# Performance work log

Hardware: AMD Instinct MI355X
Metric: run time of the kernel (lower is better)

## Reference

```python
import jax, jax.numpy as jnp
import numpy as np

B, HF, WF = 16, 32, 32
DIM, NH = 1024, 16
HD = DIM // NH  # 64


def axial_freqs(H, W, head_dim):
    # RotaryEmbedding(dim=head_dim//4, freqs_for='pixel', max_freq=H*W)
    d = head_dim // 4  # rotary dim per axis
    base = jnp.linspace(1.0, (H * W) / 2.0, d // 2) * jnp.pi  # [d//2]
    posH = jnp.linspace(-1.0, 1.0, H)
    posW = jnp.linspace(-1.0, 1.0, W)
    fH = jnp.repeat(posH[:, None] * base[None, :], 2, axis=-1)  # [H, d]
    fW = jnp.repeat(posW[:, None] * base[None, :], 2, axis=-1)  # [W, d]
    fH = jnp.broadcast_to(fH[:, None, :], (H, W, d))
    fW = jnp.broadcast_to(fW[None, :, :], (H, W, d))
    return jnp.concatenate([fH, fW], axis=-1)  # [H, W, 2d] = [H, W, head_dim//2]


def rotate_half(x):
    # interleaved pair rotation: (x1, x2) -> (-x2, x1)
    xr = x.reshape(*x.shape[:-1], -1, 2)
    x1, x2 = xr[..., 0], xr[..., 1]
    return jnp.stack([-x2, x1], axis=-1).reshape(x.shape)


def apply_rotary(freqs, t):
    # t: [B, h, H, W, hd]; freqs: [H, W, rot_dim]
    rd = freqs.shape[-1]
    t_rot, t_pass = t[..., :rd], t[..., rd:]
    t_rot = t_rot * jnp.cos(freqs) + rotate_half(t_rot) * jnp.sin(freqs)
    return jnp.concatenate([t_rot, t_pass], axis=-1)


def setup_inputs() -> dict:
    key = jax.random.key(0)
    k1, k2, k3 = jax.random.split(key, 3)
    s = 1.0 / np.sqrt(DIM)
    return {
        "x": jax.random.normal(k1, (B, HF * WF, DIM), jnp.float32),
        "w_qkv": jax.random.normal(k2, (3 * DIM, DIM), jnp.float32) * s,
        "w_proj": jax.random.normal(k3, (DIM, DIM), jnp.float32) * s,
        "b_proj": jnp.zeros((DIM,), jnp.float32),
    }


def reference(x, w_qkv, w_proj, b_proj):
    freqs = axial_freqs(HF, WF, HD)
    qkv = x @ w_qkv.T  # [B, N, 3*DIM]
    q, k, v = jnp.split(qkv, 3, axis=-1)

    def to_grid(t):  # [B, N, DIM] -> [B, h, H, W, hd]
        return t.reshape(B, HF, WF, NH, HD).transpose(0, 3, 1, 2, 4)

    q, k, v = to_grid(q), to_grid(k), to_grid(v)
    q = apply_rotary(freqs, q)
    k = apply_rotary(freqs, k)
    N = HF * WF
    q = q.reshape(B, NH, N, HD)
    k = k.reshape(B, NH, N, HD)
    v = v.reshape(B, NH, N, HD)

    scale = 1.0 / np.sqrt(HD)
    attn = jax.nn.softmax(jnp.einsum('bhnd,bhmd->bhnm', q, k) * scale, axis=-1)
    out = jnp.einsum('bhnm,bhmd->bhnd', attn, v)  # [B, h, N, hd]
    out = out.transpose(0, 2, 1, 3).reshape(B, N, DIM)
    return out @ w_proj.T + b_proj
```

## Files before the change

kernel.cpp:

```cpp
#include <hip/hip_runtime.h>
#include <hip/hip_bf16.h>
#include <math.h>

typedef __bf16 bf16;
typedef bf16 bf16x2 __attribute__((ext_vector_type(2)));
typedef bf16 bf16x4 __attribute__((ext_vector_type(4)));
typedef bf16 bf16x8 __attribute__((ext_vector_type(8)));
typedef float f32x4 __attribute__((ext_vector_type(4)));
typedef float f32x16 __attribute__((ext_vector_type(16)));
typedef unsigned int uint;
typedef uint uint32x4 __attribute__((ext_vector_type(4)));

#define MFMA16(a, b, c) __builtin_amdgcn_mfma_f32_16x16x32_bf16((a), (b), (c), 0, 0, 0)
#define MFMA32(a, b, c) __builtin_amdgcn_mfma_f32_32x32x16_bf16((a), (b), (c), 0, 0, 0)

#define QSCALE 0.18033688011112042f

__device__ __forceinline__ void async16(const void* g, void* l) {
  __builtin_amdgcn_global_load_lds(
      (const __attribute__((address_space(1))) void*)g,
      (__attribute__((address_space(3))) void*)l, 16, 0, 0);
}

__device__ __forceinline__ uint pkbf(float a, float b) {
  bf16x2 t = {(bf16)a, (bf16)b};
  return __builtin_bit_cast(uint, t);
}

__device__ __forceinline__ void pls(uint& x, uint& y) {
  asm volatile("v_permlane32_swap_b32 %0, %1" : "+v"(x), "+v"(y));
}

__global__ __launch_bounds__(256) void f2b_all_kernel(const float* __restrict__ x,
                                                      const float* __restrict__ wqkv,
                                                      const float* __restrict__ wproj,
                                                      bf16* __restrict__ xb,
                                                      bf16* __restrict__ wqb,
                                                      bf16* __restrict__ wpb) {
  int t = blockIdx.x * 256 + threadIdx.x;
  const float* in;
  bf16* out;
  int i;
  if (t < 4194304) {
    in = x; out = xb; i = t * 4;
  } else if (t < 4980736) {
    in = wqkv; out = wqb; i = (t - 4194304) * 4;
  } else {
    in = wproj; out = wpb; i = (t - 4980736) * 4;
  }
  f32x4 v = *(const f32x4*)(in + i);
  bf16x4 o = {(bf16)v[0], (bf16)v[1], (bf16)v[2], (bf16)v[3]};
  *(bf16x4*)(out + i) = o;
}

__global__ __launch_bounds__(256) void table_kernel(float* __restrict__ cosT,
                                                    float* __restrict__ sinT) {
  int idx = blockIdx.x * 256 + threadIdx.x;
  if (idx >= 1024 * 32) return;
  int n = idx >> 5, d = idx & 31;
  int hf = n >> 5, wf = n & 31;
  int bi = (d & 15) >> 1;
  float base = (1.0f + 73.0f * bi) * 3.14159265358979323846f;
  int p = (d < 16) ? hf : wf;
  float pos = (2.0f * (float)p - 31.0f) * (1.0f / 31.0f);
  float f = pos * base;
  cosT[idx] = cosf(f);
  sinT[idx] = sinf(f);
}

template <int EPI, int NBN>
__global__ __launch_bounds__(512, 2) void gemm_bt(
    const bf16* __restrict__ A, const bf16* __restrict__ W,
    bf16* __restrict__ oq, bf16* __restrict__ okk, bf16* __restrict__ ovt,
    const float* __restrict__ cosT, const float* __restrict__ sinT,
    float* __restrict__ outF, const float* __restrict__ bias) {
  constexpr int K = 1024;
  __shared__ bf16 As[4][256 * 32];
  __shared__ bf16 Bs[4][256 * 32];

  const int tid = threadIdx.x;
  const int lane = tid & 63;
  const int wid = tid >> 6;
  const int lo = lane & 15, hi = lane >> 4;
  const int wm = wid >> 2;
  const int wn = wid & 3;

  const int wg = blockIdx.x;
  const int xcd = wg & 7;
  const int i = wg >> 3;
  const int s = i >> 4;
  const int r = i & 15;
  const int bm = xcd * 8 + (s & 1) * 4 + (r & 3);
  const int bn = (s >> 1) * 4 + (r >> 2);

  const bf16* Ab = A + (size_t)bm * 256 * K;
  const bf16* Wb = W + (size_t)bn * 256 * K;

  const f32x4 fzero = {0.f, 0.f, 0.f, 0.f};
  f32x4 acc[8][4];
#pragma unroll
  for (int i2 = 0; i2 < 8; ++i2)
#pragma unroll
    for (int j = 0; j < 4; ++j) acc[i2][j] = fzero;

  size_t srcOff[2];
  int ldsOff[2];
#pragma unroll
  for (int i2 = 0; i2 < 2; ++i2) {
    const int c = i2 * 512 + tid;
    const int row = c >> 2, g = c & 3;
    const int gsrc = g ^ ((row >> 1) & 3);
    srcOff[i2] = (size_t)row * K + gsrc * 8;
    ldsOff[i2] = c * 8;
  }

  auto stageSlot = [&](int slot, int kh) {
#pragma unroll
    for (int i2 = 0; i2 < 2; ++i2)
      async16(Ab + srcOff[i2] + kh * 32, &As[slot][ldsOff[i2]]);
#pragma unroll
    for (int i2 = 0; i2 < 2; ++i2)
      async16(Wb + srcOff[i2] + kh * 32, &Bs[slot][ldsOff[i2]]);
  };

  auto compute = [&](int slot) {
    bf16x8 af[8], bf[4];
#pragma unroll
    for (int mf = 0; mf < 8; ++mf) {
      const int row = wm * 128 + mf * 16 + lo;
      const int g = hi ^ ((row >> 1) & 3);
      af[mf] = *(const bf16x8*)&As[slot][row * 32 + g * 8];
    }
#pragma unroll
    for (int nf = 0; nf < 4; ++nf) {
      const int row = wn * 64 + nf * 16 + lo;
      const int g = hi ^ ((row >> 1) & 3);
      bf[nf] = *(const bf16x8*)&Bs[slot][row * 32 + g * 8];
    }
    __builtin_amdgcn_s_setprio(1);
#pragma unroll
    for (int mf = 0; mf < 8; ++mf)
#pragma unroll
      for (int nf = 0; nf < 4; ++nf)
        acc[mf][nf] = MFMA16(af[mf], bf[nf], acc[mf][nf]);
    __builtin_amdgcn_s_setprio(0);
  };

  stageSlot(0, 0);
  stageSlot(1, 1);

  for (int kt = 0; kt < 7; ++kt) {
#pragma unroll
    for (int ph = 0; ph < 4; ++ph) {
      stageSlot((ph + 2) & 3, kt * 4 + ph + 2);
      asm volatile("s_waitcnt vmcnt(8)" ::: "memory");
      __builtin_amdgcn_s_barrier();
      compute(ph);
    }
  }
  stageSlot(2, 30);
  asm volatile("s_waitcnt vmcnt(8)" ::: "memory");
  __builtin_amdgcn_s_barrier();
  compute(0);
  stageSlot(3, 31);
  asm volatile("s_waitcnt vmcnt(8)" ::: "memory");
  __builtin_amdgcn_s_barrier();
  compute(1);
  asm volatile("s_waitcnt vmcnt(4)" ::: "memory");
  __builtin_amdgcn_s_barrier();
  compute(2);
  asm volatile("s_waitcnt vmcnt(0)" ::: "memory");
  __builtin_amdgcn_s_barrier();
  compute(3);

  const int rb0 = bm * 256 + wm * 128;
  const int jb0 = bn * 256 + wn * 64;

  if constexpr (EPI == 0) {
#pragma unroll
    for (int ac = 0; ac < 4; ++ac) {
      const int j = jb0 + ac * 16 + lo;
      const int which = j >> 10;
      const int f = j & 1023;
      const int h = f >> 6, d = f & 63;
#pragma unroll
      for (int ar = 0; ar < 8; ++ar) {
        const int rb = rb0 + ar * 16 + 4 * hi;
        f32x4 v = acc[ar][ac];
        if (which == 2) {
          const int b = rb >> 10, n0 = rb & 1023;
          bf16x4 pk = {(bf16)v[0], (bf16)v[1], (bf16)v[2], (bf16)v[3]};
          *(bf16x4*)(ovt + ((size_t)((b * 16 + h) * 64 + d)) * 1024 + n0) = pk;
        } else {
          bf16* dst = which ? okk : oq;
          const float sc = which ? 1.0f : QSCALE;
#pragma unroll
          for (int reg = 0; reg < 4; ++reg) {
            const int r2 = rb + reg;
            const int b = r2 >> 10, n = r2 & 1023;
            float val = v[reg];
            float res;
            if (d < 32) {
              float c = cosT[n * 32 + d];
              float sn = sinT[n * 32 + d];
              float pp = __shfl_xor(val, 1);
              res = (d & 1) ? fmaf(val, c, pp * sn) : fmaf(val, c, -(pp * sn));
            } else {
              res = val;
            }
            dst[((size_t)((b * 16 + h) * 1024 + n)) * 64 + d] = (bf16)(res * sc);
          }
        }
      }
    }
  } else {
#pragma unroll
    for (int ac = 0; ac < 4; ++ac) {
      const int j = jb0 + ac * 16 + lo;
      const float bv = bias[j];
#pragma unroll
      for (int ar = 0; ar < 8; ++ar) {
        const int rb = rb0 + ar * 16 + 4 * hi;
#pragma unroll
        for (int reg = 0; reg < 4; ++reg)
          outF[(size_t)(rb + reg) * 1024 + j] = acc[ar][ac][reg] + bv;
      }
    }
  }
}

__global__ __launch_bounds__(512, 4) void attn_fwd(const bf16* __restrict__ q,
                                                   const bf16* __restrict__ k,
                                                   const bf16* __restrict__ vt,
                                                   bf16* __restrict__ o) {
  __shared__ bf16 Kt[2][64 * 64];
  __shared__ bf16 Vt[2][64 * 64];
  __shared__ float Psm[8][32];
  const int tid = threadIdx.x;
  const int lane = tid & 63, wid = tid >> 6;
  const int l31 = lane & 31;
  const int s = lane >> 5;
  const int m7 = l31 & 7;
  const int j = blockIdx.x;
  const int bh = (j & 7) + ((j >> 5) << 3);
  const int qt = (j >> 3) & 3;
  const bf16* qg = q + (size_t)bh * 65536;
  const bf16* kg = k + (size_t)bh * 65536;
  const bf16* vg = vt + (size_t)bh * 65536;

  const int qrow = qt * 256 + wid * 32 + l31;
  bf16x8 qf[4];
#pragma unroll
  for (int kb4 = 0; kb4 < 4; ++kb4)
    qf[kb4] = *(const bf16x8*)(qg + (size_t)qrow * 64 + kb4 * 16 + s * 8);

  const int srow = tid >> 3;
  const int sgsrc = (tid & 7) ^ (srow & 7);
  auto stageKV = [&](int buf, int kv) {
    async16(kg + (size_t)(kv * 64 + srow) * 64 + sgsrc * 8, &Kt[buf][tid * 8]);
    async16(vg + (size_t)srow * 1024 + kv * 64 + sgsrc * 8, &Vt[buf][tid * 8]);
  };

  asm volatile("s_waitcnt vmcnt(0)" ::: "memory");
  stageKV(0, 0);

  f32x16 of0 = {0.f, 0.f, 0.f, 0.f, 0.f, 0.f, 0.f, 0.f,
                0.f, 0.f, 0.f, 0.f, 0.f, 0.f, 0.f, 0.f};
  f32x16 of1 = of0;
  float psum = 0.f;

  for (int kv = 0; kv < 16; ++kv) {
    const int cur = kv & 1;
    if (kv < 15) {
      stageKV(cur ^ 1, kv + 1);
      asm volatile("s_waitcnt vmcnt(2)" ::: "memory");
    } else {
      asm volatile("s_waitcnt vmcnt(0)" ::: "memory");
    }
    __builtin_amdgcn_s_barrier();

    f32x16 z0 = {0.f, 0.f, 0.f, 0.f, 0.f, 0.f, 0.f, 0.f,
                 0.f, 0.f, 0.f, 0.f, 0.f, 0.f, 0.f, 0.f};
    f32x16 z1 = z0;
#pragma unroll
    for (int kb4 = 0; kb4 < 4; ++kb4) {
      bf16x8 k0 = *(const bf16x8*)&Kt[cur][l31 * 64 + (((2 * kb4 + s) ^ m7) * 8)];
      bf16x8 k1 = *(const bf16x8*)&Kt[cur][(32 + l31) * 64 + (((2 * kb4 + s) ^ m7) * 8)];
      z0 = MFMA32(k0, qf[kb4], z0);
      z1 = MFMA32(k1, qf[kb4], z1);
    }

    uint c0[8], c1[8];
#pragma unroll
    for (int m = 0; m < 8; ++m) {
      float a0 = __builtin_amdgcn_exp2f(z0[2 * m]);
      float b0 = __builtin_amdgcn_exp2f(z0[2 * m + 1]);
      float a1 = __builtin_amdgcn_exp2f(z1[2 * m]);
      float b1 = __builtin_amdgcn_exp2f(z1[2 * m + 1]);
      psum += (a0 + b0) + (a1 + b1);
      c0[m] = pkbf(a0, b0);
      c1[m] = pkbf(a1, b1);
    }

    auto pv = [&](uint* cc, int bb, int kb) {
      uint w0 = cc[4 * bb], w2 = cc[4 * bb + 2];
      uint w1 = cc[4 * bb + 1], w3 = cc[4 * bb + 3];
      pls(w0, w2);
      pls(w1, w3);
      uint32x4 W = {w0, w1, w2, w3};
      bf16x8 apv = __builtin_bit_cast(bf16x8, W);
      bf16x8 vb0 = *(const bf16x8*)&Vt[cur][l31 * 64 + (((2 * kb + s) ^ m7) * 8)];
      bf16x8 vb1 = *(const bf16x8*)&Vt[cur][(32 + l31) * 64 + (((2 * kb + s) ^ m7) * 8)];
      of0 = MFMA32(apv, vb0, of0);
      of1 = MFMA32(apv, vb1, of1);
    };
    pv(c0, 0, 0);
    pv(c0, 1, 1);
    pv(c1, 0, 2);
    pv(c1, 1, 3);

    __syncthreads();
  }

  psum += __shfl_xor(psum, 32);
  const float inv = 1.0f / psum;
  if (lane < 32) Psm[wid][l31] = inv;
  __syncthreads();

  const int b = bh >> 4, h = bh & 15;
#pragma unroll
  for (int r = 0; r < 16; ++r) {
    const int qr = (r & 3) + 8 * (r >> 2) + 4 * s;
    const float iv = Psm[wid][qr];
    const int n = qt * 256 + wid * 32 + qr;
    const size_t base = ((size_t)(b * 1024 + n)) * 1024 + h * 64 + l31;
    o[base] = (bf16)(of0[r] * iv);
    o[base + 32] = (bf16)(of1[r] * iv);
  }
}

extern "C" void kernel_launch(void* const* d_in, const int* in_sizes, int n_in,
                              void* d_out, int out_size, void* d_ws, size_t ws_size,
                              hipStream_t stream) {
  (void)in_sizes; (void)n_in; (void)out_size; (void)ws_size;
  const float* x = (const float*)d_in[0];
  const float* wqkv = (const float*)d_in[1];
  const float* wproj = (const float*)d_in[2];
  const float* bproj = (const float*)d_in[3];

  char* ws = (char*)d_ws;
  bf16* xb = (bf16*)(ws);
  bf16* wqb = (bf16*)(ws + 33554432);
  bf16* wpb = (bf16*)(ws + 39845888);
  float* cosT = (float*)(ws + 41943040);
  float* sinT = (float*)(ws + 42074112);
  bf16* qb = (bf16*)(ws + 42205184);
  bf16* kb = (bf16*)(ws + 75759616);
  bf16* vtb = (bf16*)(ws + 109314048);

  f2b_all_kernel<<<20480, 256, 0, stream>>>(x, wqkv, wproj, xb, wqb, wpb);
  table_kernel<<<128, 256, 0, stream>>>(cosT, sinT);

  gemm_bt<0, 12><<<768, 512, 0, stream>>>(xb, wqb, qb, kb, vtb, cosT, sinT,
                                          nullptr, nullptr);
  attn_fwd<<<1024, 512, 0, stream>>>(qb, kb, vtb, xb);
  gemm_bt<1, 4><<<256, 512, 0, stream>>>(xb, wpb, nullptr, nullptr, nullptr,
                                         nullptr, nullptr, (float*)d_out, bproj);
}
```

Baseline: 253.8 us.

## Switch GEMM mainloop to double-buffered BK=64 stages with wider swizzle

Replaces the four-slot, 32-wide K pipeline (prefetch distance 2) with two 64-wide K slots and a prefetch distance of 1. Each stage now issues twice as many async loads and runs two MFMA sub-steps, and the LDS XOR swizzle is changed to an 8-group pattern. There are half as many barrier phases, but a second barrier is added per iteration to guard slot reuse. Less load-latency hiding is the risk. The shared-memory footprint stays the same.

```diff
diff --git a/kernel.cpp b/kernel.cpp
--- a/kernel.cpp
+++ b/kernel.cpp
@@ -75,8 +75,8 @@
     const float* __restrict__ cosT, const float* __restrict__ sinT,
     float* __restrict__ outF, const float* __restrict__ bias) {
   constexpr int K = 1024;
-  __shared__ bf16 As[4][256 * 32];
-  __shared__ bf16 Bs[4][256 * 32];
+  __shared__ bf16 As[2][256 * 64];
+  __shared__ bf16 Bs[2][256 * 64];
 
   const int tid = threadIdx.x;
   const int lane = tid & 63;
@@ -88,10 +88,10 @@
   const int wg = blockIdx.x;
   const int xcd = wg & 7;
   const int i = wg >> 3;
-  const int s = i >> 4;
-  const int r = i & 15;
-  const int bm = xcd * 8 + (s & 1) * 4 + (r & 3);
-  const int bn = (s >> 1) * 4 + (r >> 2);
+  const int s4 = i >> 4;
+  const int r4 = i & 15;
+  const int bm = xcd * 8 + (s4 & 1) * 4 + (r4 & 3);
+  const int bn = (s4 >> 1) * 4 + (r4 >> 2);
 
   const bf16* Ab = A + (size_t)bm * 256 * K;
   const bf16* Wb = W + (size_t)bn * 256 * K;
@@ -103,75 +103,64 @@
 #pragma unroll
     for (int j = 0; j < 4; ++j) acc[i2][j] = fzero;
 
-  size_t srcOff[2];
-  int ldsOff[2];
-#pragma unroll
-  for (int i2 = 0; i2 < 2; ++i2) {
+  size_t srcOff[4];
+  int ldsOff[4];
+#pragma unroll
+  for (int i2 = 0; i2 < 4; ++i2) {
     const int c = i2 * 512 + tid;
-    const int row = c >> 2, g = c & 3;
-    const int gsrc = g ^ ((row >> 1) & 3);
+    const int row = c >> 3, g = c & 7;
+    const int gsrc = g ^ (row & 7);
     srcOff[i2] = (size_t)row * K + gsrc * 8;
     ldsOff[i2] = c * 8;
   }
 
-  auto stageSlot = [&](int slot, int kh) {
-#pragma unroll
-    for (int i2 = 0; i2 < 2; ++i2)
-      async16(Ab + srcOff[i2] + kh * 32, &As[slot][ldsOff[i2]]);
-#pragma unroll
-    for (int i2 = 0; i2 < 2; ++i2)
-      async16(Wb + srcOff[i2] + kh * 32, &Bs[slot][ldsOff[i2]]);
+  auto stageSlot = [&](int slot, int kt) {
+#pragma unroll
+    for (int i2 = 0; i2 < 4; ++i2)
+      async16(Ab + srcOff[i2] + kt * 64, &As[slot][ldsOff[i2]]);
+#pragma unroll
+    for (int i2 = 0; i2 < 4; ++i2)
+      async16(Wb + srcOff[i2] + kt * 64, &Bs[slot][ldsOff[i2]]);
   };
 
   auto compute = [&](int slot) {
-    bf16x8 af[8], bf[4];
-#pragma unroll
-    for (int mf = 0; mf < 8; ++mf) {
-      const int row = wm * 128 + mf * 16 + lo;
-      const int g = hi ^ ((row >> 1) & 3);
-      af[mf] = *(const bf16x8*)&As[slot][row * 32 + g * 8];
-    }
-#pragma unroll
-    for (int nf = 0; nf < 4; ++nf) {
-      const int row = wn * 64 + nf * 16 + lo;
-      const int g = hi ^ ((row >> 1) & 3);
-      bf[nf] = *(const bf16x8*)&Bs[slot][row * 32 + g * 8];
-    }
-    __builtin_amdgcn_s_setprio(1);
-#pragma unroll
-    for (int mf = 0; mf < 8; ++mf)
-#pragma unroll
-      for (int nf = 0; nf < 4; ++nf)
-        acc[mf][nf] = MFMA16(af[mf], bf[nf], acc[mf][nf]);
-    __builtin_amdgcn_s_setprio(0);
+#pragma unroll
+    for (int s = 0; s < 2; ++s) {
+      bf16x8 af[8], bf[4];
+#pragma unroll
+      for (int mf = 0; mf < 8; ++mf) {
+        const int row = wm * 128 + mf * 16 + lo;
+        const int g = (s * 4 + hi) ^ (row & 7);
+        af[mf] = *(const bf16x8*)&As[slot][row * 64 + g * 8];
+      }
+#pragma unroll
+      for (int nf = 0; nf < 4; ++nf) {
+        const int row = wn * 64 + nf * 16 + lo;
+        const int g = (s * 4 + hi) ^ (row & 7);
+        bf[nf] = *(const bf16x8*)&Bs[slot][row * 64 + g * 8];
+      }
+      __builtin_amdgcn_s_setprio(1);
+#pragma unroll
+      for (int mf = 0; mf < 8; ++mf)
+#pragma unroll
+        for (int nf = 0; nf < 4; ++nf)
+          acc[mf][nf] = MFMA16(af[mf], bf[nf], acc[mf][nf]);
+      __builtin_amdgcn_s_setprio(0);
+    }
   };
 
   stageSlot(0, 0);
-  stageSlot(1, 1);
-
-  for (int kt = 0; kt < 7; ++kt) {
-#pragma unroll
-    for (int ph = 0; ph < 4; ++ph) {
-      stageSlot((ph + 2) & 3, kt * 4 + ph + 2);
-      asm volatile("s_waitcnt vmcnt(8)" ::: "memory");
-      __builtin_amdgcn_s_barrier();
-      compute(ph);
-    }
-  }
-  stageSlot(2, 30);
-  asm volatile("s_waitcnt vmcnt(8)" ::: "memory");
-  __builtin_amdgcn_s_barrier();
-  compute(0);
-  stageSlot(3, 31);
-  asm volatile("s_waitcnt vmcnt(8)" ::: "memory");
+
+  for (int p = 0; p < 15; ++p) {
+    stageSlot((p + 1) & 1, p + 1);
+    asm volatile("s_waitcnt vmcnt(8)" ::: "memory");
+    __builtin_amdgcn_s_barrier();
+    compute(p & 1);
+    __builtin_amdgcn_s_barrier();
+  }
+  asm volatile("s_waitcnt vmcnt(0)" ::: "memory");
   __builtin_amdgcn_s_barrier();
   compute(1);
-  asm volatile("s_waitcnt vmcnt(4)" ::: "memory");
-  __builtin_amdgcn_s_barrier();
-  compute(2);
-  asm volatile("s_waitcnt vmcnt(0)" ::: "memory");
-  __builtin_amdgcn_s_barrier();
-  compute(3);
 
   const int rb0 = bm * 256 + wm * 128;
   const int jb0 = bn * 256 + wn * 64;
```

After: 264.3 us. +4.1%, slower.

## Process 64 query rows per wave in attention to reuse K/V tiles

Applied to the files above, without the earlier changes.

Each wave in the attention kernel now handles two 32-row query slices instead of one, so every K and V fragment read from LDS feeds twice as many MFMAs. The grid is halved to 512 blocks of 512 query rows, which halves the global K/V staging traffic per query. In exchange register use roughly doubles (launch bounds lowered to 2 blocks per CU), occupancy drops, and fewer blocks are available to fill the GPU.

```diff
diff --git a/kernel.cpp b/kernel.cpp
--- a/kernel.cpp
+++ b/kernel.cpp
@@ -229,30 +229,33 @@
   }
 }
 
-__global__ __launch_bounds__(512, 4) void attn_fwd(const bf16* __restrict__ q,
+__global__ __launch_bounds__(512, 2) void attn_fwd(const bf16* __restrict__ q,
                                                    const bf16* __restrict__ k,
                                                    const bf16* __restrict__ vt,
                                                    bf16* __restrict__ o) {
   __shared__ bf16 Kt[2][64 * 64];
   __shared__ bf16 Vt[2][64 * 64];
-  __shared__ float Psm[8][32];
+  __shared__ float Psm[8][64];
   const int tid = threadIdx.x;
   const int lane = tid & 63, wid = tid >> 6;
   const int l31 = lane & 31;
   const int s = lane >> 5;
   const int m7 = l31 & 7;
   const int j = blockIdx.x;
-  const int bh = (j & 7) + ((j >> 5) << 3);
-  const int qt = (j >> 3) & 3;
+  const int bh = (j & 7) + ((j >> 4) << 3);
+  const int qt = (j >> 3) & 1;
   const bf16* qg = q + (size_t)bh * 65536;
   const bf16* kg = k + (size_t)bh * 65536;
   const bf16* vg = vt + (size_t)bh * 65536;
 
-  const int qrow = qt * 256 + wid * 32 + l31;
-  bf16x8 qf[4];
-#pragma unroll
-  for (int kb4 = 0; kb4 < 4; ++kb4)
-    qf[kb4] = *(const bf16x8*)(qg + (size_t)qrow * 64 + kb4 * 16 + s * 8);
+  bf16x8 qf[2][4];
+#pragma unroll
+  for (int rs = 0; rs < 2; ++rs) {
+    const int qrow = qt * 512 + wid * 64 + rs * 32 + l31;
+#pragma unroll
+    for (int kb4 = 0; kb4 < 4; ++kb4)
+      qf[rs][kb4] = *(const bf16x8*)(qg + (size_t)qrow * 64 + kb4 * 16 + s * 8);
+  }
 
   const int srow = tid >> 3;
   const int sgsrc = (tid & 7) ^ (srow & 7);
@@ -264,10 +267,10 @@
   asm volatile("s_waitcnt vmcnt(0)" ::: "memory");
   stageKV(0, 0);
 
-  f32x16 of0 = {0.f, 0.f, 0.f, 0.f, 0.f, 0.f, 0.f, 0.f,
-                0.f, 0.f, 0.f, 0.f, 0.f, 0.f, 0.f, 0.f};
-  f32x16 of1 = of0;
-  float psum = 0.f;
+  const f32x16 z16 = {0.f, 0.f, 0.f, 0.f, 0.f, 0.f, 0.f, 0.f,
+                      0.f, 0.f, 0.f, 0.f, 0.f, 0.f, 0.f, 0.f};
+  f32x16 of00 = z16, of01 = z16, of10 = z16, of11 = z16;
+  float psum0 = 0.f, psum1 = 0.f;
 
   for (int kv = 0; kv < 16; ++kv) {
     const int cur = kv & 1;
@@ -279,63 +282,84 @@
     }
     __builtin_amdgcn_s_barrier();
 
-    f32x16 z0 = {0.f, 0.f, 0.f, 0.f, 0.f, 0.f, 0.f, 0.f,
-                 0.f, 0.f, 0.f, 0.f, 0.f, 0.f, 0.f, 0.f};
-    f32x16 z1 = z0;
+    f32x16 z00 = z16, z01 = z16, z10 = z16, z11 = z16;
 #pragma unroll
     for (int kb4 = 0; kb4 < 4; ++kb4) {
       bf16x8 k0 = *(const bf16x8*)&Kt[cur][l31 * 64 + (((2 * kb4 + s) ^ m7) * 8)];
       bf16x8 k1 = *(const bf16x8*)&Kt[cur][(32 + l31) * 64 + (((2 * kb4 + s) ^ m7) * 8)];
-      z0 = MFMA32(k0, qf[kb4], z0);
-      z1 = MFMA32(k1, qf[kb4], z1);
-    }
-
-    uint c0[8], c1[8];
+      z00 = MFMA32(k0, qf[0][kb4], z00);
+      z01 = MFMA32(k1, qf[0][kb4], z01);
+      z10 = MFMA32(k0, qf[1][kb4], z10);
+      z11 = MFMA32(k1, qf[1][kb4], z11);
+    }
+
+    uint c00[8], c01[8], c10[8], c11[8];
 #pragma unroll
     for (int m = 0; m < 8; ++m) {
-      float a0 = __builtin_amdgcn_exp2f(z0[2 * m]);
-      float b0 = __builtin_amdgcn_exp2f(z0[2 * m + 1]);
-      float a1 = __builtin_amdgcn_exp2f(z1[2 * m]);
-      float b1 = __builtin_amdgcn_exp2f(z1[2 * m + 1]);
-      psum += (a0 + b0) + (a1 + b1);
-      c0[m] = pkbf(a0, b0);
-      c1[m] = pkbf(a1, b1);
-    }
-
-    auto pv = [&](uint* cc, int bb, int kb) {
-      uint w0 = cc[4 * bb], w2 = cc[4 * bb + 2];
-      uint w1 = cc[4 * bb + 1], w3 = cc[4 * bb + 3];
+      float a, b;
+      a = __builtin_amdgcn_exp2f(z00[2 * m]); b = __builtin_amdgcn_exp2f(z00[2 * m + 1]);
+      psum0 += a + b; c00[m] = pkbf(a, b);
+      a = __builtin_amdgcn_exp2f(z01[2 * m]); b = __builtin_amdgcn_exp2f(z01[2 * m + 1]);
+      psum0 += a + b; c01[m] = pkbf(a, b);
+      a = __builtin_amdgcn_exp2f(z10[2 * m]); b = __builtin_amdgcn_exp2f(z10[2 * m + 1]);
+      psum1 += a + b; c10[m] = pkbf(a, b);
+      a = __builtin_amdgcn_exp2f(z11[2 * m]); b = __builtin_amdgcn_exp2f(z11[2 * m + 1]);
+      psum1 += a + b; c11[m] = pkbf(a, b);
+    }
+
+    auto pv2 = [&](const uint* cA, const uint* cB, int bb, int kb) {
+      bf16x8 vb0 = *(const bf16x8*)&Vt[cur][l31 * 64 + (((2 * kb + s) ^ m7) * 8)];
+      bf16x8 vb1 = *(const bf16x8*)&Vt[cur][(32 + l31) * 64 + (((2 * kb + s) ^ m7) * 8)];
+      uint w0 = cA[4 * bb], w2 = cA[4 * bb + 2];
+      uint w1 = cA[4 * bb + 1], w3 = cA[4 * bb + 3];
       pls(w0, w2);
       pls(w1, w3);
-      uint32x4 W = {w0, w1, w2, w3};
-      bf16x8 apv = __builtin_bit_cast(bf16x8, W);
-      bf16x8 vb0 = *(const bf16x8*)&Vt[cur][l31 * 64 + (((2 * kb + s) ^ m7) * 8)];
-      bf16x8 vb1 = *(const bf16x8*)&Vt[cur][(32 + l31) * 64 + (((2 * kb + s) ^ m7) * 8)];
-      of0 = MFMA32(apv, vb0, of0);
-      of1 = MFMA32(apv, vb1, of1);
+      uint32x4 WA = {w0, w1, w2, w3};
+      bf16x8 apv0 = __builtin_bit_cast(bf16x8, WA);
+      of00 = MFMA32(apv0, vb0, of00);
+      of01 = MFMA32(apv0, vb1, of01);
+      uint y0 = cB[4 * bb], y2 = cB[4 * bb + 2];
+      uint y1 = cB[4 * bb + 1], y3 = cB[4 * bb + 3];
+      pls(y0, y2);
+      pls(y1, y3);
+      uint32x4 WB = {y0, y1, y2, y3};
+      bf16x8 apv1 = __builtin_bit_cast(bf16x8, WB);
+      of10 = MFMA32(apv1, vb0, of10);
+      of11 = MFMA32(apv1, vb1, of11);
     };
-    pv(c0, 0, 0);
-    pv(c0, 1, 1);
-    pv(c1, 0, 2);
-    pv(c1, 1, 3);
+    pv2(c00, c10, 0, 0);
+    pv2(c00, c10, 1, 1);
+    pv2(c01, c11, 0, 2);
+    pv2(c01, c11, 1, 3);
 
     __syncthreads();
   }
 
-  psum += __shfl_xor(psum, 32);
-  const float inv = 1.0f / psum;
-  if (lane < 32) Psm[wid][l31] = inv;
+  psum0 += __shfl_xor(psum0, 32);
+  psum1 += __shfl_xor(psum1, 32);
+  if (lane < 32) {
+    Psm[wid][l31] = 1.0f / psum0;
+    Psm[wid][32 + l31] = 1.0f / psum1;
+  }
   __syncthreads();
 
   const int b = bh >> 4, h = bh & 15;
 #pragma unroll
-  for (int r = 0; r < 16; ++r) {
-    const int qr = (r & 3) + 8 * (r >> 2) + 4 * s;
-    const float iv = Psm[wid][qr];
-    const int n = qt * 256 + wid * 32 + qr;
-    const size_t base = ((size_t)(b * 1024 + n)) * 1024 + h * 64 + l31;
-    o[base] = (bf16)(of0[r] * iv);
-    o[base + 32] = (bf16)(of1[r] * iv);
+  for (int rs = 0; rs < 2; ++rs) {
+#pragma unroll
+    for (int r = 0; r < 16; ++r) {
+      const int qr = (r & 3) + 8 * (r >> 2) + 4 * s;
+      const float iv = Psm[wid][rs * 32 + qr];
+      const int n = qt * 512 + wid * 64 + rs * 32 + qr;
+      const size_t base = ((size_t)(b * 1024 + n)) * 1024 + h * 64 + l31;
+      if (rs == 0) {
+        o[base] = (bf16)(of00[r] * iv);
+        o[base + 32] = (bf16)(of01[r] * iv);
+      } else {
+        o[base] = (bf16)(of10[r] * iv);
+        o[base + 32] = (bf16)(of11[r] * iv);
+      }
+    }
   }
 }
 
@@ -363,7 +387,7 @@
 
   gemm_bt<0, 12><<<768, 512, 0, stream>>>(xb, wqb, qb, kb, vtb, cosT, sinT,
                                           nullptr, nullptr);
-  attn_fwd<<<1024, 512, 0, stream>>>(qb, kb, vtb, xb);
+  attn_fwd<<<512, 512, 0, stream>>>(qb, kb, vtb, xb);
   gemm_bt<1, 4><<<256, 512, 0, stream>>>(xb, wpb, nullptr, nullptr, nullptr,
                                          nullptr, nullptr, (float*)d_out, bproj);
 }
```

After: 258.1 us. No clear change (+1.7%).
